# Kernel tuning notes

Measured on AMD Instinct MI355X. Metric: run time of the kernel, lower is better.

## Reference

```python
import jax, jax.numpy as jnp
import numpy as np

PI = np.pi
DOWN = 4          # down_ratio
K = 50            # max_detection
DET_THRES = 0.29
IN_W, IN_H = 1920, 1056

DIM_MEAN = jnp.array([
    (3.99331126, 1.54370861, 1.64175497), (0.295, 1.6, 0.3175),
    (1.34645161, 1.55322581, 0.3883871), (2.503, 1.72, 1.077),
    (9.1775, 2.95, 2.3425), (10.3655102, 3.31632653, 2.45469388),
    (6.016911083, 3.412001685, 2.2783185), (4.824963, 2.046904, 1.78939),
    (8.8040879, 2.916193, 2.07649252)], dtype=jnp.float32)
ALPHA_CENTERS = jnp.array([0.0, PI / 2, PI, -PI / 2], dtype=jnp.float32)


def nms_hm(heat, kernel=5):
    pad = (kernel - 1) // 2
    hmax = jax.lax.reduce_window(heat, -jnp.inf, jax.lax.max,
                                 (1, 1, kernel, kernel), (1, 1, 1, 1),
                                 [(0, 0), (0, 0), (pad, pad), (pad, pad)])
    return jnp.where(hmax == heat, heat, 0.0)


def select_topk(heat, k):
    B, C, H, W = heat.shape
    sc_all, ind_all = jax.lax.top_k(heat.reshape(B, C, H * W), k)   # [B,C,K]
    ys_all = (ind_all // W).astype(jnp.float32)
    xs_all = (ind_all % W).astype(jnp.float32)
    sc, ind = jax.lax.top_k(sc_all.reshape(B, C * k), k)            # [B,K]
    cls = (ind // k).astype(jnp.float32)
    g = lambda t: jnp.take_along_axis(t.reshape(B, C * k), ind, axis=1)
    return sc, g(ind_all), cls, g(ys_all), g(xs_all)


def setup_inputs() -> dict:
    key = jax.random.key(0)
    k1, k2 = jax.random.split(key)
    output_cls = jax.random.uniform(k1, (16, 9, 264, 480), dtype=jnp.float32)
    output_regs = jax.random.normal(k2, (16, 46, 264, 480), dtype=jnp.float32)
    # KITTI P2-style projection matrix
    calib = jnp.array([[721.5377, 0.0, 609.5593, 44.85728],
                       [0.0, 721.5377, 172.854, 0.2163791],
                       [0.0, 0.0, 1.0, 0.00274588]], dtype=jnp.float32)
    return {"output_cls": output_cls, "output_regs": output_regs, "calib": calib}


def reference(output_cls, output_regs, calib):
    B, C, H, W = output_cls.shape
    heat = nms_hm(output_cls, 5)
    scores, inds, clses, ys, xs = select_topk(heat, K)
    scores = scores.reshape(-1)        # [N], N = B*K
    inds = inds.reshape(-1)            # flattened spatial index < H*W
    clses = clses.reshape(-1)
    pts = jnp.stack([xs.reshape(-1), ys.reshape(-1)], axis=1)  # [N,2]

    Ch = output_regs.shape[1]
    regs = output_regs.reshape(B, Ch, H * W).transpose(0, 2, 1)  # [B,HW,Ch]
    pois = jnp.take_along_axis(regs, inds.reshape(B, K)[..., None], axis=1).reshape(-1, Ch)

    # validity: score threshold, then dedup by spatial index keeping the
    # entry with max class id (first occurrence), matching del_dul_id(clses, indexs)
    thresh = scores >= DET_THRES
    pos = jnp.arange(scores.shape[0], dtype=jnp.float32)
    keyv = jnp.where(thresh, clses * 1e4 - pos, -jnp.inf)
    segmax = jax.ops.segment_max(keyv, inds, num_segments=H * W)
    valid = thresh & (keyv == segmax[inds])

    reg2d = jax.nn.relu(pois[:, 0:4])
    off3d = pois[:, 4:6]
    dims_off = pois[:, 22:25]
    ori = jnp.concatenate([pois[:, 25:33], pois[:, 33:41]], axis=1)  # [N,16]
    depth_off = pois[:, 41]

    center = pts + off3d
    box2d = jnp.concatenate([center - reg2d[:, :2], center + reg2d[:, 2:]], axis=1) * DOWN
    box2d = jnp.stack([jnp.clip(box2d[:, 0], 0, IN_W), jnp.clip(box2d[:, 1], 0, IN_H),
                       jnp.clip(box2d[:, 2], 0, IN_W), jnp.clip(box2d[:, 3], 0, IN_H)], axis=1)

    cls_id = clses.astype(jnp.int32)
    dims = jnp.exp(dims_off) * DIM_MEAN[cls_id]               # dim_modes=['exp',True,False]
    depth = jnp.clip(1.0 / jax.nn.sigmoid(depth_off) - 1.0, 0.1, 200.0)

    # project_image_to_rect
    pimg = center * DOWN
    fu, cu, fv, cv = calib[0, 0], calib[0, 2], calib[1, 1], calib[1, 2]
    bx = calib[0, 3] / (-fu)
    by = calib[1, 3] / (-fv)
    locx = (pimg[:, 0] - cu) * depth / fu + bx
    locy = (pimg[:, 1] - cv) * depth / fv + by
    locs = jnp.stack([locx, locy, depth], axis=1)

    # multibin orientation
    bin_cls = jax.nn.softmax(ori[:, :8].reshape(-1, 4, 2), axis=2)[..., 1]
    b = jnp.argmax(bin_cls, axis=1)                           # [N]
    off = ori[:, 8:16].reshape(-1, 4, 2)
    sel = jnp.take_along_axis(off, b[:, None, None], axis=1)[:, 0, :]  # [N,2]
    alphas = jnp.arctan(sel[:, 0] / sel[:, 1]) + ALPHA_CENTERS[b]
    rays = jnp.arctan(locs[:, 0] / locs[:, 2])
    rotys = alphas + rays
    rotys = jnp.where(rotys > PI, rotys - 2 * PI, rotys)
    rotys = jnp.where(rotys < -PI, rotys + 2 * PI, rotys)
    alphas = jnp.where(alphas > PI, alphas - 2 * PI, alphas)
    alphas = jnp.where(alphas < -PI, alphas + 2 * PI, alphas)

    out = jnp.concatenate([box2d, dims, depth[:, None], locs,
                           rotys[:, None], alphas[:, None], scores[:, None]], axis=1)  # [N,14]
    return out, valid, cls_id
```

## Files before the change

### kernel.cpp

```cpp
#include <hip/hip_runtime.h>
#include <math.h>

#define Hd 264
#define Wd 480
#define HW (Hd * Wd)
#define NB 16
#define NC 9
#define KK 50
#define NPLANE (NB * NC)
#define NDET (NB * KK)
#define CAP 6912
#define K1CH 8
#define F4PC (HW / 4 / K1CH)
#define SLAB_CAP 512
#define SCAP 1024
#define TB_F 0.998f
#define PI_F 3.14159274101257324f
#define TWO_PI_F 6.28318548202514648f

__device__ const float DIMM[9][3] = {
    {3.99331126f, 1.54370861f, 1.64175497f},
    {0.295f, 1.6f, 0.3175f},
    {1.34645161f, 1.55322581f, 0.3883871f},
    {2.503f, 1.72f, 1.077f},
    {9.1775f, 2.95f, 2.3425f},
    {10.3655102f, 3.31632653f, 2.45469388f},
    {6.016911083f, 3.412001685f, 2.2783185f},
    {4.824963f, 2.046904f, 1.78939f},
    {8.8040879f, 2.916193f, 2.07649252f}};

__device__ const float ACENT[4] = {0.0f, 1.57079637050628662f, 3.14159274101257324f, -1.57079637050628662f};

__device__ __forceinline__ unsigned long long mkkey(float v, unsigned int idx) {
    return ((unsigned long long)__float_as_uint(v) << 32) | (unsigned long long)(0xFFFFFFFFu - idx);
}

__global__ __launch_bounds__(256) void thresh_scan(const float* __restrict__ cls,
                                                   unsigned long long* __restrict__ slabs,
                                                   int* __restrict__ slabCnt,
                                                   int* __restrict__ batchCnt) {
    __shared__ unsigned long long sbuf[SLAB_CAP];
    __shared__ int scnt;

    const int plane = blockIdx.y;
    const int chunk = blockIdx.x;
    const int tid = threadIdx.x;
    if (tid == 0) {
        scnt = 0;
        if (chunk == 0 && plane < NB) batchCnt[plane] = 0;
    }
    __syncthreads();

    const float4* hp4 = (const float4*)(cls + (size_t)plane * HW) + (size_t)chunk * F4PC;
    const unsigned int base = (unsigned int)(chunk * F4PC * 4);

    for (int q = tid; q < F4PC; q += 256) {
        const float4 v = hp4[q];
        const unsigned int i0 = base + 4u * (unsigned int)q;
        if (v.x >= TB_F) { const int p = atomicAdd(&scnt, 1); if (p < SLAB_CAP) sbuf[p] = mkkey(v.x, i0); }
        if (v.y >= TB_F) { const int p = atomicAdd(&scnt, 1); if (p < SLAB_CAP) sbuf[p] = mkkey(v.y, i0 + 1); }
        if (v.z >= TB_F) { const int p = atomicAdd(&scnt, 1); if (p < SLAB_CAP) sbuf[p] = mkkey(v.z, i0 + 2); }
        if (v.w >= TB_F) { const int p = atomicAdd(&scnt, 1); if (p < SLAB_CAP) sbuf[p] = mkkey(v.w, i0 + 3); }
    }
    __syncthreads();
    const int n = min(scnt, SLAB_CAP);
    unsigned long long* dst = slabs + (size_t)(plane * K1CH + chunk) * SLAB_CAP;
    for (int j = tid; j < n; j += 256) dst[j] = sbuf[j];
    if (tid == 0) slabCnt[plane * K1CH + chunk] = scnt;
}

__global__ __launch_bounds__(256) void select_topk(const float* __restrict__ cls,
                                                   const unsigned long long* __restrict__ slabs,
                                                   const int* __restrict__ slabCnt,
                                                   unsigned long long* __restrict__ planeKeys,
                                                   int* __restrict__ batchCnt,
                                                   float* __restrict__ dScore,
                                                   int* __restrict__ dInd,
                                                   int* __restrict__ dCls) {
    __shared__ unsigned long long candG[CAP];
    __shared__ unsigned long long S[SCAP];
    __shared__ unsigned int sidx[NC * KK];
    __shared__ int soff[K1CH + 1];
    __shared__ int s_scnt, s_over, s_last;
    __shared__ unsigned long long wmax_[4];
    __shared__ unsigned long long sprev;

    const int plane = blockIdx.x;
    const int tid = threadIdx.x;
    const float* hp = cls + (size_t)plane * HW;

    if (tid == 0) { s_scnt = 0; s_over = 0; }
    __syncthreads();
    if (tid < K1CH) {
        const int c = slabCnt[plane * K1CH + tid];
        soff[tid + 1] = min(c, SLAB_CAP);
        if (c > SLAB_CAP) atomicAdd(&s_over, 1);
    }
    __syncthreads();
    if (tid == 0) {
        soff[0] = 0;
        for (int c = 1; c <= K1CH; ++c) soff[c] += soff[c - 1];
    }
    __syncthreads();
    const int n = soff[K1CH];

    for (int j = tid; j < n; j += 256) {
        int lo = 0, hi = K1CH;
        while (hi - lo > 1) { const int mid = (lo + hi) >> 1; if (soff[mid] <= j) lo = mid; else hi = mid; }
        candG[j] = slabs[(size_t)(plane * K1CH + lo) * SLAB_CAP + (j - soff[lo])];
    }
    __syncthreads();

    for (int j = tid; j < n; j += 256) {
        const unsigned long long k = candG[j];
        const unsigned int idx = 0xFFFFFFFFu - (unsigned int)(k & 0xFFFFFFFFull);
        const float v = __uint_as_float((unsigned int)(k >> 32));
        const int y = (int)idx / Wd, x = (int)idx - ((int)idx / Wd) * Wd;
        const int ylo = max(y - 2, 0), yhi = min(y + 2, Hd - 1);
        const int xlo = max(x - 2, 0), xhi = min(x + 2, Wd - 1);
        float wm = -INFINITY;
        for (int yy = ylo; yy <= yhi; ++yy)
            for (int xx = xlo; xx <= xhi; ++xx)
                wm = fmaxf(wm, hp[yy * Wd + xx]);
        if (v == wm) {
            const int p = atomicAdd(&s_scnt, 1);
            if (p < SCAP) S[p] = k;
        }
    }
    __syncthreads();
    const int sc = s_scnt;

    if (s_over == 0 && sc >= KK && sc <= SCAP) {
        for (int idx = tid; idx < sc; idx += 256) {
            const unsigned long long k = S[idx];
            int r = 0;
            for (int j = 0; j < sc; ++j) r += (S[j] > k) ? 1 : 0;
            if (r < KK) planeKeys[plane * KK + r] = k;
        }
    } else {
        if (tid == 0) s_scnt = 0;
        for (int j = tid; j < KK; j += 256) planeKeys[plane * KK + j] = 0;
        __syncthreads();
        for (int px = tid; px < HW; px += 256) {
            const float v = hp[px];
            const int y = px / Wd, x = px - (px / Wd) * Wd;
            const int ylo = max(y - 2, 0), yhi = min(y + 2, Hd - 1);
            const int xlo = max(x - 2, 0), xhi = min(x + 2, Wd - 1);
            float wm = -INFINITY;
            for (int yy = ylo; yy <= yhi; ++yy)
                for (int xx = xlo; xx <= xhi; ++xx)
                    wm = fmaxf(wm, hp[yy * Wd + xx]);
            if (v == wm) {
                const int p = atomicAdd(&s_scnt, 1);
                if (p < CAP) candG[p] = mkkey(v, (unsigned int)px);
            }
        }
        __syncthreads();
        const int nn = min(s_scnt, CAP);
        unsigned long long prev = ~0ull;
        for (int it = 0; it < KK; ++it) {
            unsigned long long mk = 0;
            for (int j = tid; j < nn; j += 256) {
                unsigned long long k = candG[j];
                if (k == prev) { candG[j] = 0; k = 0; }
                if (k > mk) mk = k;
            }
            for (int s = 32; s > 0; s >>= 1) {
                const unsigned long long o = __shfl_down(mk, s);
                if (o > mk) mk = o;
            }
            if ((tid & 63) == 0) wmax_[tid >> 6] = mk;
            __syncthreads();
            if (tid == 0) {
                unsigned long long m = wmax_[0];
                if (wmax_[1] > m) m = wmax_[1];
                if (wmax_[2] > m) m = wmax_[2];
                if (wmax_[3] > m) m = wmax_[3];
                planeKeys[plane * KK + it] = m;
                sprev = m;
            }
            __syncthreads();
            prev = sprev;
        }
    }

    __threadfence();
    __syncthreads();
    if (tid == 0) s_last = (atomicAdd(&batchCnt[plane / NC], 1) == NC - 1) ? 1 : 0;
    __syncthreads();
    if (!s_last) return;
    __threadfence();

    const int b = plane / NC;
    for (int j = tid; j < NC * KK; j += 256) {
        const unsigned long long pk = planeKeys[(b * NC + j / KK) * KK + (j % KK)];
        sidx[j] = 0xFFFFFFFFu - (unsigned int)(pk & 0xFFFFFFFFull);
        S[j] = (pk & 0xFFFFFFFF00000000ull) | (unsigned long long)(0xFFFFFFFFu - (unsigned int)j);
    }
    __syncthreads();
    for (int idx = tid; idx < NC * KK; idx += 256) {
        const unsigned long long k = S[idx];
        int r = 0;
        for (int j = 0; j < NC * KK; ++j) r += (S[j] > k) ? 1 : 0;
        if (r < KK) {
            dScore[b * KK + r] = __uint_as_float((unsigned int)(k >> 32));
            dInd[b * KK + r] = (int)sidx[idx];
            dCls[b * KK + r] = idx / KK;
        }
    }
}

__global__ __launch_bounds__(64) void finalize(const float* __restrict__ regs,
                                               const float* __restrict__ calib,
                                               const float* __restrict__ dScore,
                                               const int* __restrict__ dInd,
                                               const int* __restrict__ dCls,
                                               float* __restrict__ out) {
    __shared__ float s[26];
    const int i = blockIdx.x;
    const int lane = threadIdx.x;
    const int ind0 = dInd[i];
    const int ind = (ind0 >= 0 && ind0 < HW) ? ind0 : 0;
    const int b = i / KK;

    if (lane < 26) {
        const int ch = (lane < 6) ? lane : lane + 16;
        s[lane] = regs[(size_t)b * 46 * HW + (size_t)ch * HW + (size_t)ind];
    }

    float m = -INFINITY;
    for (int j = lane; j < NDET; j += 64) {
        if (dInd[j] == ind0 && dScore[j] >= 0.29f) {
            m = fmaxf(m, (float)dCls[j] * 10000.0f - (float)j);
        }
    }
#pragma unroll
    for (int sft = 32; sft > 0; sft >>= 1) m = fmaxf(m, __shfl_down(m, sft));
    __syncthreads();
    if (lane != 0) return;

    const int cls = dCls[i];
    const float score = dScore[i];
    const bool th = score >= 0.29f;
    const float key_i = th ? (float)cls * 10000.0f - (float)i : -INFINITY;
    const bool valid = th && (key_i == m);

    const float x = (float)(ind % Wd);
    const float y = (float)(ind / Wd);

    const float r0 = fmaxf(s[0], 0.0f), r1 = fmaxf(s[1], 0.0f);
    const float r2 = fmaxf(s[2], 0.0f), r3 = fmaxf(s[3], 0.0f);
    const float cx = x + s[4];
    const float cy = y + s[5];

    const float bx1 = fminf(fmaxf((cx - r0) * 4.0f, 0.0f), 1920.0f);
    const float by1 = fminf(fmaxf((cy - r1) * 4.0f, 0.0f), 1056.0f);
    const float bx2 = fminf(fmaxf((cx + r2) * 4.0f, 0.0f), 1920.0f);
    const float by2 = fminf(fmaxf((cy + r3) * 4.0f, 0.0f), 1056.0f);

    const float dim0 = expf(s[6]) * DIMM[cls][0];
    const float dim1 = expf(s[7]) * DIMM[cls][1];
    const float dim2 = expf(s[8]) * DIMM[cls][2];

    const float sig = 1.0f / (1.0f + expf(-s[25]));
    const float depth = fminf(fmaxf(1.0f / sig - 1.0f, 0.1f), 200.0f);

    const float fu = calib[0], cu = calib[2], fv = calib[5], cv = calib[6];
    const float bxo = calib[3] / -fu;
    const float byo = calib[7] / -fv;
    const float locx = (cx * 4.0f - cu) * depth / fu + bxo;
    const float locy = (cy * 4.0f - cv) * depth / fv + byo;

    float best = -INFINITY;
    int bidx = 0;
#pragma unroll
    for (int t = 0; t < 4; ++t) {
        const float l0 = s[9 + 2 * t], l1 = s[9 + 2 * t + 1];
        const float mm = fmaxf(l0, l1);
        const float p1 = expf(l1 - mm) / (expf(l0 - mm) + expf(l1 - mm));
        if (p1 > best) { best = p1; bidx = t; }
    }
    const float sel0 = s[17 + 2 * bidx], sel1 = s[17 + 2 * bidx + 1];
    float alpha = atanf(sel0 / sel1) + ACENT[bidx];
    const float ray = atanf(locx / depth);
    float roty = alpha + ray;
    if (roty > PI_F) roty -= TWO_PI_F;
    if (roty < -PI_F) roty += TWO_PI_F;
    if (alpha > PI_F) alpha -= TWO_PI_F;
    if (alpha < -PI_F) alpha += TWO_PI_F;

    float* o = out + (size_t)i * 14;
    o[0] = bx1; o[1] = by1; o[2] = bx2; o[3] = by2;
    o[4] = dim0; o[5] = dim1; o[6] = dim2;
    o[7] = depth;
    o[8] = locx; o[9] = locy; o[10] = depth;
    o[11] = roty; o[12] = alpha;
    o[13] = score;
    out[NDET * 14 + i] = valid ? 1.0f : 0.0f;
    out[NDET * 15 + i] = (float)cls;
}

extern "C" void kernel_launch(void* const* d_in, const int* in_sizes, int n_in,
                              void* d_out, int out_size, void* d_ws, size_t ws_size,
                              hipStream_t stream) {
    const float* cls = (const float*)d_in[0];
    const float* regs = (const float*)d_in[1];
    const float* calib = (const float*)d_in[2];
    float* out = (float*)d_out;
    char* ws = (char*)d_ws;

    int* slabCnt = (int*)ws;
    unsigned long long* slabs = (unsigned long long*)(ws + 32768);
    char* tail = ws + 32768 + 4718592;
    unsigned long long* planeKeys = (unsigned long long*)tail;
    float* dScore = (float*)(tail + 57600);
    int* dInd = (int*)(tail + 60800);
    int* dCls = (int*)(tail + 64000);
    int* batchCnt = (int*)(tail + 67200);

    hipLaunchKernelGGL(thresh_scan, dim3(K1CH, NPLANE), dim3(256), 0, stream, cls, slabs, slabCnt, batchCnt);
    hipLaunchKernelGGL(select_topk, dim3(NPLANE), dim3(256), 0, stream, cls, slabs, slabCnt,
                       planeKeys, batchCnt, dScore, dInd, dCls);
    hipLaunchKernelGGL(finalize, dim3(NDET), dim3(64), 0, stream, regs, calib, dScore, dInd, dCls, out);
}
```

Baseline: 61.50 us.

## Split batch top-k into separate kernel and move fallback buffer to global memory

The last-block-done batch merge (atomic counter plus threadfences) is removed from select_topk and replaced by a separate batch_topk kernel launched per batch. The large shared candidate array used only by the fallback path moves to a global scratch buffer, which cuts select_topk's shared memory so more blocks can be resident per CU. The per-candidate NMS check now reads slab keys straight from global memory instead of staging them in shared memory. The cost is one extra kernel launch, and the rarely used fallback path becomes slower because it works out of global memory.

```diff
diff --git a/kernel.cpp b/kernel.cpp
--- a/kernel.cpp
+++ b/kernel.cpp
@@ -7,13 +7,14 @@
 #define NB 16
 #define NC 9
 #define KK 50
-#define NPLANE (NB * NC)
-#define NDET (NB * KK)
-#define CAP 6912
+#define NPLANE 144
+#define NDET 800
+#define NK 450
 #define K1CH 8
 #define F4PC (HW / 4 / K1CH)
 #define SLAB_CAP 512
 #define SCAP 1024
+#define FB_CAP 16384
 #define TB_F 0.998f
 #define PI_F 3.14159274101257324f
 #define TWO_PI_F 6.28318548202514648f
@@ -37,18 +38,14 @@
 
 __global__ __launch_bounds__(256) void thresh_scan(const float* __restrict__ cls,
                                                    unsigned long long* __restrict__ slabs,
-                                                   int* __restrict__ slabCnt,
-                                                   int* __restrict__ batchCnt) {
+                                                   int* __restrict__ slabCnt) {
     __shared__ unsigned long long sbuf[SLAB_CAP];
     __shared__ int scnt;
 
     const int plane = blockIdx.y;
     const int chunk = blockIdx.x;
     const int tid = threadIdx.x;
-    if (tid == 0) {
-        scnt = 0;
-        if (chunk == 0 && plane < NB) batchCnt[plane] = 0;
-    }
+    if (tid == 0) scnt = 0;
     __syncthreads();
 
     const float4* hp4 = (const float4*)(cls + (size_t)plane * HW) + (size_t)chunk * F4PC;
@@ -73,26 +70,23 @@
                                                    const unsigned long long* __restrict__ slabs,
                                                    const int* __restrict__ slabCnt,
                                                    unsigned long long* __restrict__ planeKeys,
-                                                   int* __restrict__ batchCnt,
-                                                   float* __restrict__ dScore,
-                                                   int* __restrict__ dInd,
-                                                   int* __restrict__ dCls) {
-    __shared__ unsigned long long candG[CAP];
+                                                   unsigned long long* __restrict__ fbBuf,
+                                                   int* __restrict__ fbCnt) {
     __shared__ unsigned long long S[SCAP];
-    __shared__ unsigned int sidx[NC * KK];
     __shared__ int soff[K1CH + 1];
-    __shared__ int s_scnt, s_over, s_last;
-    __shared__ unsigned long long wmax_[4];
+    __shared__ int s_scnt, s_over;
+    __shared__ unsigned long long wmax[4];
     __shared__ unsigned long long sprev;
 
-    const int plane = blockIdx.x;
+    const int p = blockIdx.x;
     const int tid = threadIdx.x;
-    const float* hp = cls + (size_t)plane * HW;
+    const int lane = tid & 63, wid = tid >> 6;
+    const float* hp = cls + (size_t)p * HW;
 
     if (tid == 0) { s_scnt = 0; s_over = 0; }
     __syncthreads();
     if (tid < K1CH) {
-        const int c = slabCnt[plane * K1CH + tid];
+        const int c = slabCnt[p * K1CH + tid];
         soff[tid + 1] = min(c, SLAB_CAP);
         if (c > SLAB_CAP) atomicAdd(&s_over, 1);
     }
@@ -104,18 +98,46 @@
     __syncthreads();
     const int n = soff[K1CH];
 
-    for (int j = tid; j < n; j += 256) {
-        int lo = 0, hi = K1CH;
-        while (hi - lo > 1) { const int mid = (lo + hi) >> 1; if (soff[mid] <= j) lo = mid; else hi = mid; }
-        candG[j] = slabs[(size_t)(plane * K1CH + lo) * SLAB_CAP + (j - soff[lo])];
-    }
-    __syncthreads();
-
-    for (int j = tid; j < n; j += 256) {
-        const unsigned long long k = candG[j];
-        const unsigned int idx = 0xFFFFFFFFu - (unsigned int)(k & 0xFFFFFFFFull);
-        const float v = __uint_as_float((unsigned int)(k >> 32));
-        const int y = (int)idx / Wd, x = (int)idx - ((int)idx / Wd) * Wd;
+    if (!s_over) {
+        for (int j = tid; j < n; j += 256) {
+            int lo = 0, hi = K1CH;
+            while (hi - lo > 1) { const int mid = (lo + hi) >> 1; if (soff[mid] <= j) lo = mid; else hi = mid; }
+            const unsigned long long k = slabs[(size_t)(p * K1CH + lo) * SLAB_CAP + (j - soff[lo])];
+            const unsigned int idx = 0xFFFFFFFFu - (unsigned int)(k & 0xFFFFFFFFull);
+            const float v = __uint_as_float((unsigned int)(k >> 32));
+            const int y = (int)idx / Wd, x = (int)idx - ((int)idx / Wd) * Wd;
+            const int ylo = max(y - 2, 0), yhi = min(y + 2, Hd - 1);
+            const int xlo = max(x - 2, 0), xhi = min(x + 2, Wd - 1);
+            float wm = -INFINITY;
+            for (int yy = ylo; yy <= yhi; ++yy)
+                for (int xx = xlo; xx <= xhi; ++xx)
+                    wm = fmaxf(wm, hp[yy * Wd + xx]);
+            if (v == wm) {
+                const int q = atomicAdd(&s_scnt, 1);
+                if (q < SCAP) S[q] = k;
+            }
+        }
+    }
+    __syncthreads();
+    const int sc = s_scnt;
+
+    if (!s_over && sc >= KK && sc <= SCAP) {
+        for (int idx = tid; idx < sc; idx += 256) {
+            const unsigned long long k = S[idx];
+            int r = 0;
+            for (int j = 0; j < sc; ++j) r += (S[j] > k) ? 1 : 0;
+            if (r < KK) planeKeys[p * KK + r] = k;
+        }
+        return;
+    }
+
+    if (tid == 0) fbCnt[p] = 0;
+    for (int j = tid; j < KK; j += 256) planeKeys[p * KK + j] = 0;
+    __syncthreads();
+    unsigned long long* fb = fbBuf + (size_t)p * FB_CAP;
+    for (int px = tid; px < HW; px += 256) {
+        const float v = hp[px];
+        const int y = px / Wd, x = px - (px / Wd) * Wd;
         const int ylo = max(y - 2, 0), yhi = min(y + 2, Hd - 1);
         const int xlo = max(x - 2, 0), xhi = min(x + 2, Wd - 1);
         float wm = -INFINITY;
@@ -123,85 +145,58 @@
             for (int xx = xlo; xx <= xhi; ++xx)
                 wm = fmaxf(wm, hp[yy * Wd + xx]);
         if (v == wm) {
-            const int p = atomicAdd(&s_scnt, 1);
-            if (p < SCAP) S[p] = k;
-        }
-    }
-    __syncthreads();
-    const int sc = s_scnt;
-
-    if (s_over == 0 && sc >= KK && sc <= SCAP) {
-        for (int idx = tid; idx < sc; idx += 256) {
-            const unsigned long long k = S[idx];
-            int r = 0;
-            for (int j = 0; j < sc; ++j) r += (S[j] > k) ? 1 : 0;
-            if (r < KK) planeKeys[plane * KK + r] = k;
-        }
-    } else {
-        if (tid == 0) s_scnt = 0;
-        for (int j = tid; j < KK; j += 256) planeKeys[plane * KK + j] = 0;
+            const int q = atomicAdd(&fbCnt[p], 1);
+            if (q < FB_CAP) fb[q] = mkkey(v, (unsigned int)px);
+        }
+    }
+    __syncthreads();
+    const int nn = min(fbCnt[p], FB_CAP);
+    unsigned long long prevk = ~0ull;
+    for (int it = 0; it < KK; ++it) {
+        unsigned long long mk = 0;
+        for (int j = tid; j < nn; j += 256) {
+            unsigned long long k = fb[j];
+            if (k == prevk) { fb[j] = 0; k = 0; }
+            if (k > mk) mk = k;
+        }
+        for (int s = 32; s > 0; s >>= 1) {
+            const unsigned long long o = __shfl_down(mk, s);
+            if (o > mk) mk = o;
+        }
+        if (lane == 0) wmax[wid] = mk;
         __syncthreads();
-        for (int px = tid; px < HW; px += 256) {
-            const float v = hp[px];
-            const int y = px / Wd, x = px - (px / Wd) * Wd;
-            const int ylo = max(y - 2, 0), yhi = min(y + 2, Hd - 1);
-            const int xlo = max(x - 2, 0), xhi = min(x + 2, Wd - 1);
-            float wm = -INFINITY;
-            for (int yy = ylo; yy <= yhi; ++yy)
-                for (int xx = xlo; xx <= xhi; ++xx)
-                    wm = fmaxf(wm, hp[yy * Wd + xx]);
-            if (v == wm) {
-                const int p = atomicAdd(&s_scnt, 1);
-                if (p < CAP) candG[p] = mkkey(v, (unsigned int)px);
-            }
+        if (tid == 0) {
+            unsigned long long m = wmax[0];
+            if (wmax[1] > m) m = wmax[1];
+            if (wmax[2] > m) m = wmax[2];
+            if (wmax[3] > m) m = wmax[3];
+            planeKeys[p * KK + it] = m;
+            sprev = m;
         }
         __syncthreads();
-        const int nn = min(s_scnt, CAP);
-        unsigned long long prev = ~0ull;
-        for (int it = 0; it < KK; ++it) {
-            unsigned long long mk = 0;
-            for (int j = tid; j < nn; j += 256) {
-                unsigned long long k = candG[j];
-                if (k == prev) { candG[j] = 0; k = 0; }
-                if (k > mk) mk = k;
-            }
-            for (int s = 32; s > 0; s >>= 1) {
-                const unsigned long long o = __shfl_down(mk, s);
-                if (o > mk) mk = o;
-            }
-            if ((tid & 63) == 0) wmax_[tid >> 6] = mk;
-            __syncthreads();
-            if (tid == 0) {
-                unsigned long long m = wmax_[0];
-                if (wmax_[1] > m) m = wmax_[1];
-                if (wmax_[2] > m) m = wmax_[2];
-                if (wmax_[3] > m) m = wmax_[3];
-                planeKeys[plane * KK + it] = m;
-                sprev = m;
-            }
-            __syncthreads();
-            prev = sprev;
-        }
-    }
-
-    __threadfence();
-    __syncthreads();
-    if (tid == 0) s_last = (atomicAdd(&batchCnt[plane / NC], 1) == NC - 1) ? 1 : 0;
-    __syncthreads();
-    if (!s_last) return;
-    __threadfence();
-
-    const int b = plane / NC;
-    for (int j = tid; j < NC * KK; j += 256) {
-        const unsigned long long pk = planeKeys[(b * NC + j / KK) * KK + (j % KK)];
+        prevk = sprev;
+    }
+}
+
+__global__ __launch_bounds__(256) void batch_topk(const unsigned long long* __restrict__ planeKeys,
+                                                  float* __restrict__ dScore, int* __restrict__ dInd,
+                                                  int* __restrict__ dCls) {
+    __shared__ unsigned long long k2[NK];
+    __shared__ unsigned int sidx[NK];
+
+    const int b = blockIdx.x;
+    const int tid = threadIdx.x;
+    for (int j = tid; j < NK; j += 256) {
+        const unsigned long long pk = planeKeys[b * NK + j];
         sidx[j] = 0xFFFFFFFFu - (unsigned int)(pk & 0xFFFFFFFFull);
-        S[j] = (pk & 0xFFFFFFFF00000000ull) | (unsigned long long)(0xFFFFFFFFu - (unsigned int)j);
-    }
-    __syncthreads();
-    for (int idx = tid; idx < NC * KK; idx += 256) {
-        const unsigned long long k = S[idx];
+        k2[j] = (pk & 0xFFFFFFFF00000000ull) | (unsigned long long)(0xFFFFFFFFu - (unsigned int)j);
+    }
+    __syncthreads();
+
+    for (int idx = tid; idx < NK; idx += 256) {
+        const unsigned long long k = k2[idx];
         int r = 0;
-        for (int j = 0; j < NC * KK; ++j) r += (S[j] > k) ? 1 : 0;
+        for (int j = 0; j < NK; ++j) r += (k2[j] > k) ? 1 : 0;
         if (r < KK) {
             dScore[b * KK + r] = __uint_as_float((unsigned int)(k >> 32));
             dInd[b * KK + r] = (int)sidx[idx];
@@ -310,16 +305,17 @@
     char* ws = (char*)d_ws;
 
     int* slabCnt = (int*)ws;
-    unsigned long long* slabs = (unsigned long long*)(ws + 32768);
-    char* tail = ws + 32768 + 4718592;
-    unsigned long long* planeKeys = (unsigned long long*)tail;
-    float* dScore = (float*)(tail + 57600);
-    int* dInd = (int*)(tail + 60800);
-    int* dCls = (int*)(tail + 64000);
-    int* batchCnt = (int*)(tail + 67200);
-
-    hipLaunchKernelGGL(thresh_scan, dim3(K1CH, NPLANE), dim3(256), 0, stream, cls, slabs, slabCnt, batchCnt);
+    int* fbCnt = (int*)(ws + 8192);
+    unsigned long long* planeKeys = (unsigned long long*)(ws + 16384);
+    float* dScore = (float*)(ws + 73984);
+    int* dInd = (int*)(ws + 77184);
+    int* dCls = (int*)(ws + 80384);
+    unsigned long long* slabs = (unsigned long long*)(ws + 98304);
+    unsigned long long* fbBuf = (unsigned long long*)(ws + 98304 + 4718592);
+
+    hipLaunchKernelGGL(thresh_scan, dim3(K1CH, NPLANE), dim3(256), 0, stream, cls, slabs, slabCnt);
     hipLaunchKernelGGL(select_topk, dim3(NPLANE), dim3(256), 0, stream, cls, slabs, slabCnt,
-                       planeKeys, batchCnt, dScore, dInd, dCls);
+                       planeKeys, fbBuf, fbCnt);
+    hipLaunchKernelGGL(batch_topk, dim3(NB), dim3(256), 0, stream, planeKeys, dScore, dInd, dCls);
     hipLaunchKernelGGL(finalize, dim3(NDET), dim3(64), 0, stream, regs, calib, dScore, dInd, dCls, out);
 }
```

Result: faster. 59.39 us, median of 2 (-3.4%).
